# Performance work log

Hardware: AMD Instinct MI355X
Metric: run time of the kernel (lower is better)

Reference implementation:

```python
import jax, jax.numpy as jnp
import numpy as np
from jax import lax
from jax.scipy.special import logsumexp

TRIGGER_SIZE = 34
NTAG = TRIGGER_SIZE + 2  # +START/STOP
START = TRIGGER_SIZE
STOP = TRIGGER_SIZE + 1


def setup_inputs() -> dict:
    key = jax.random.key(0)
    k1, k2, k3, k4, k5 = jax.random.split(key, 5)
    B, S, H = 64, 512, 768
    x_1 = jax.random.normal(k1, (B, S, H), dtype=jnp.float32)
    head_indexes = jax.random.randint(k2, (B, S), 0, S)
    triggers_y = jax.random.randint(k3, (B, S), 0, TRIGGER_SIZE)
    W = jax.random.normal(k4, (H, NTAG), dtype=jnp.float32) * (1.0 / np.sqrt(H))
    b = jnp.zeros((NTAG,), dtype=jnp.float32)
    transitions = jax.random.normal(k5, (NTAG, NTAG), dtype=jnp.float32) * 0.1
    return {"x_1": x_1, "head_indexes": head_indexes, "triggers_y": triggers_y,
            "W": W, "b": b, "transitions": transitions}


def crf_nll(emit, mask, tags, trans):
    # emit [B,S,T], mask [B,S] bool, tags [B,S], trans [T,T] (from->to)
    B, S, T = emit.shape
    maskf = mask.astype(emit.dtype)
    # --- partition (forward algorithm) ---
    alpha0 = emit[:, 0] + trans[START][None, :]  # [B,T]; pos 0 always valid

    def fstep(alpha, inp):
        e_t, m_t = inp  # [B,T], [B]
        new = logsumexp(alpha[:, :, None] + trans[None, :, :], axis=1) + e_t
        return jnp.where(m_t[:, None], new, alpha), None

    alpha, _ = lax.scan(fstep, alpha0,
                        (emit[:, 1:].transpose(1, 0, 2), mask[:, 1:].T))
    logZ = logsumexp(alpha + trans[:, STOP][None, :], axis=1)  # [B]
    # --- gold path score ---
    emit_g = jnp.take_along_axis(emit, tags[:, :, None], axis=2)[..., 0]  # [B,S]
    emit_score = (emit_g * maskf).sum(axis=1)
    trans_pair = trans[tags[:, :-1], tags[:, 1:]]  # [B,S-1]
    trans_score = (trans_pair * maskf[:, 1:]).sum(axis=1)
    xlen = mask.sum(axis=1)  # [B]
    last_tag = jnp.take_along_axis(tags, (xlen - 1)[:, None], axis=1)[:, 0]
    gold = emit_score + trans[START, tags[:, 0]] + trans_score + trans[last_tag, STOP]
    return jnp.sum(logZ - gold)


def crf_viterbi(emit, mask, trans):
    B, S, T = emit.shape
    ids = jnp.arange(T)
    delta0 = emit[:, 0] + trans[START][None, :]

    def vstep(delta, inp):
        e_t, m_t = inp
        scores = delta[:, :, None] + trans[None, :, :]  # [B,T,T]
        best = scores.max(axis=1) + e_t
        bp = jnp.argmax(scores, axis=1)  # [B,T]
        new_delta = jnp.where(m_t[:, None], best, delta)
        bp = jnp.where(m_t[:, None], bp, ids[None, :])  # identity on pad
        return new_delta, bp

    delta, bps = lax.scan(vstep, delta0,
                          (emit[:, 1:].transpose(1, 0, 2), mask[:, 1:].T))
    final = delta + trans[:, STOP][None, :]
    last_tag = jnp.argmax(final, axis=1)  # [B]
    path_score = jnp.max(final, axis=1)

    def back(tag_next, bp_t):
        tag_t = jnp.take_along_axis(bp_t, tag_next[:, None], axis=1)[:, 0]
        return tag_t, tag_t

    _, prev_tags = lax.scan(back, last_tag, bps, reverse=True)  # [S-1,B]
    path = jnp.concatenate([prev_tags.T, last_tag[:, None]], axis=1)  # [B,S]
    path = jnp.where(mask, path, 0)
    return path_score, path


def reference(x_1, head_indexes, triggers_y, W, b, transitions):
    B, S, H = x_1.shape
    # batched version of the per-sample index_select loop
    x = jnp.take_along_axis(x_1, head_indexes[:, :, None], axis=1)  # [B,S,H]
    xlen = head_indexes.max(axis=1)  # xlen = [max(row) for row in head_indexes]
    mask = jnp.arange(S)[None, :] < xlen[:, None]  # [B,S] bool
    logits = jax.nn.leaky_relu(x @ W + b)  # tri_fc1 + leaky_relu (dropout=eval)
    trigger_loss = crf_nll(logits, mask, triggers_y, transitions)
    path_score, trigger_hat = crf_viterbi(logits, mask, transitions)
    return trigger_loss, trigger_hat, path_score
```

## Files before the change

kernel.cpp:

```cpp
#include <hip/hip_runtime.h>
#include <math.h>

#define SB 64
#define SS 512
#define SH 768
#define NT 36
#define TSTART 34
#define TSTOP 35
#define NC 32
#define CL 16

#define CFENCE() asm volatile("" ::: "memory")

__device__ __forceinline__ float wave_max_f(float v) {
#pragma unroll
    for (int off = 32; off > 0; off >>= 1) v = fmaxf(v, __shfl_xor(v, off, 64));
    return v;
}
__device__ __forceinline__ float wave_sum_f(float v) {
#pragma unroll
    for (int off = 32; off > 0; off >>= 1) v += __shfl_xor(v, off, 64);
    return v;
}
__device__ __forceinline__ float bcast0(float v) {
    return __uint_as_float(__builtin_amdgcn_readfirstlane(__float_as_uint(v)));
}

#define XP 129
#define XBUF 8256
#define RED(qq, rr, jj) smem[(qq) * 2368 + (rr) * 37 + (jj)]

extern "C" __global__ __launch_bounds__(512) void k_emit(
    const float* __restrict__ x1, const int* __restrict__ hidx,
    const float* __restrict__ W, const float* __restrict__ bias,
    float* __restrict__ emit)
{
    __shared__ __align__(16) float smem[18944];

    int tid  = threadIdx.x;
    int lane = tid & 63;
    int q    = __builtin_amdgcn_readfirstlane(tid >> 6);

    int srow = tid >> 3;
    int c8   = tid & 7;
    int grs  = blockIdx.x * 64 + srow;
    int bs   = grs >> 9;
    const float4* srcRow = (const float4*)(x1 + (size_t)(bs * SS + hidx[grs]) * SH);
    int woff = srow * XP + c8 * 4;

    float acc[NT];
#pragma unroll
    for (int j = 0; j < NT; ++j) acc[j] = 0.f;

    float4 n0, n1, n2, n3;
    n0 = srcRow[c8];  n1 = srcRow[c8 + 8];
    n2 = srcRow[c8 + 16]; n3 = srcRow[c8 + 24];
    {
        float* d = smem + woff;
        d[0] = n0.x; d[1] = n0.y; d[2] = n0.z; d[3] = n0.w;
        d[32] = n1.x; d[33] = n1.y; d[34] = n1.z; d[35] = n1.w;
        d[64] = n2.x; d[65] = n2.y; d[66] = n2.z; d[67] = n2.w;
        d[96] = n3.x; d[97] = n3.y; d[98] = n3.z; d[99] = n3.w;
    }

#pragma unroll
    for (int s = 0; s < 6; ++s) {
        if (s < 5) {
            int f0 = (s + 1) * 32 + c8;
            n0 = srcRow[f0]; n1 = srcRow[f0 + 8];
            n2 = srcRow[f0 + 16]; n3 = srcRow[f0 + 24];
        }
        __syncthreads();
        {
            const float* xs = smem + (s & 1) * XBUF + lane * XP + 16 * q;
            const float* Ws = W + (size_t)(128 * s + 16 * q) * NT;
#pragma unroll
            for (int k = 0; k < 16; ++k) {
                float xv = xs[k];
                const float* wr = Ws + k * NT;
#pragma unroll
                for (int j = 0; j < NT; ++j) acc[j] += xv * wr[j];
            }
        }
        if (s < 5) {
            float* d = smem + ((s + 1) & 1) * XBUF + woff;
            d[0] = n0.x; d[1] = n0.y; d[2] = n0.z; d[3] = n0.w;
            d[32] = n1.x; d[33] = n1.y; d[34] = n1.z; d[35] = n1.w;
            d[64] = n2.x; d[65] = n2.y; d[66] = n2.z; d[67] = n2.w;
            d[96] = n3.x; d[97] = n3.y; d[98] = n3.z; d[99] = n3.w;
        }
    }
    __syncthreads();

#pragma unroll
    for (int j = 0; j < NT; ++j) RED(q, lane, j) = acc[j];
    __syncthreads();

    int r = tid >> 2, g = tid & 3;
    float vout[9];
    if (tid < 256) {
#pragma unroll
        for (int jj = 0; jj < 9; ++jj) {
            int j = g * 9 + jj;
            float v = bias[j];
#pragma unroll
            for (int qq = 0; qq < 8; ++qq) v += RED(qq, r, j);
            vout[jj] = v > 0.f ? v : 0.01f * v;
        }
    }
    __syncthreads();
    if (tid < 256) {
#pragma unroll
        for (int jj = 0; jj < 9; ++jj) smem[r * NT + g * 9 + jj] = vout[jj];
    }
    __syncthreads();
    {
        const float4* st4 = (const float4*)smem;
        float4* op = (float4*)(emit + (size_t)blockIdx.x * 64 * NT);
        for (int i = tid; i < 576; i += 512) op[i] = st4[i];
    }
}

#define LSE_STEP(T)                                                       \
    {                                                                     \
        float e_t = elsw[((T) - t0s) * NT + jj];                          \
        float m = bcast0(alpha);                                          \
        float p = __expf(alpha - m);                                      \
        bc[lane] = p;                                                     \
        CFENCE();                                                         \
        __builtin_amdgcn_wave_barrier();                                  \
        float s0 = 0.f, s1 = 0.f, s2 = 0.f, s3 = 0.f;                     \
        _Pragma("unroll")                                                 \
        for (int k = 0; k < 9; ++k) {                                     \
            float4 pv = bc4[w][k];                                        \
            s0 += pv.x * Ecol[4 * k];                                     \
            s1 += pv.y * Ecol[4 * k + 1];                                 \
            s2 += pv.z * Ecol[4 * k + 2];                                 \
            s3 += pv.w * Ecol[4 * k + 3];                                 \
        }                                                                 \
        CFENCE();                                                         \
        float anew = m + __logf((s0 + s1) + (s2 + s3)) + e_t;             \
        alpha = act ? anew : -1e30f;                                      \
    }

#define VIT_STEP(T, WRITEBP)                                              \
    {                                                                     \
        float e_t = elsw[((T) - t0s) * NT + jj];                          \
        bc[lane] = alpha;                                                 \
        CFENCE();                                                         \
        __builtin_amdgcn_wave_barrier();                                  \
        float b0 = -1e30f, b1 = -1e30f, b2 = -1e30f, b3 = -1e30f;         \
        int   i0 = 0, i1 = 1, i2 = 2, i3 = 3;                             \
        _Pragma("unroll")                                                 \
        for (int k = 0; k < 9; ++k) {                                     \
            float4 dv = bc4[w][k];                                        \
            float c0 = dv.x + tcol[4 * k];                                 \
            float c1 = dv.y + tcol[4 * k + 1];                             \
            float c2 = dv.z + tcol[4 * k + 2];                             \
            float c3 = dv.w + tcol[4 * k + 3];                             \
            if (c0 > b0) { b0 = c0; i0 = 4 * k; }                         \
            if (c1 > b1) { b1 = c1; i1 = 4 * k + 1; }                     \
            if (c2 > b2) { b2 = c2; i2 = 4 * k + 2; }                     \
            if (c3 > b3) { b3 = c3; i3 = 4 * k + 3; }                     \
        }                                                                 \
        CFENCE();                                                         \
        float best = b0; int bi = i0;                                     \
        if (b1 > best || (b1 == best && i1 < bi)) { best = b1; bi = i1; } \
        if (b2 > best || (b2 == best && i2 < bi)) { best = b2; bi = i2; } \
        if (b3 > best || (b3 == best && i3 < bi)) { best = b3; bi = i3; } \
        float dnew = best + e_t;                                          \
        alpha = act ? dnew : -1e30f;                                      \
        if ((WRITEBP) && act)                                             \
            bp[((size_t)b * SS + (T)) * 64 + jj] = (unsigned char)bi;     \
    }

extern "C" __global__ __launch_bounds__(256) void k_scan(
    const float* __restrict__ emit, const int* __restrict__ hidx,
    const float* __restrict__ trans,
    float* __restrict__ Warr, float* __restrict__ Earr,
    float* __restrict__ lse_local,
    float* __restrict__ score_local, int* __restrict__ ltag,
    unsigned char* __restrict__ bp)
{
    __shared__ float trl[NT * NT];
    __shared__ float els[4][1024];
    __shared__ float4 bc4[4][16];

    int tid  = threadIdx.x;
    int lane = tid & 63;
    int w    = __builtin_amdgcn_readfirstlane(tid >> 6);

    int wid  = blockIdx.x * 4 + w;
    int kind = wid >> 11;
    int rem  = wid & 2047;
    int b    = rem >> 5;
    int c    = rem & 31;

    const float* eb  = emit + (size_t)b * SS * NT;
    int t0s = (c > 0) ? (c * CL - 9) : 0;
    const float* ebase = eb + (size_t)t0s * NT;
    float* elsw = els[w];

#pragma unroll
    for (int i = 0; i < 4; ++i) {
        __builtin_amdgcn_global_load_lds(
            (const __attribute__((address_space(1))) void*)(ebase + i * 256 + lane * 4),
            (__attribute__((address_space(3))) void*)(elsw + i * 256), 16, 0, 0);
    }
    for (int i = tid; i < NT * NT; i += 256) trl[i] = trans[i];

    int  jj  = lane < NT ? lane : NT - 1;
    bool act = lane < NT;

    int xm = 0;
    const int* hb = hidx + b * SS;
#pragma unroll
    for (int k = 0; k < SS / 64; ++k) xm = max(xm, hb[lane + 64 * k]);
#pragma unroll
    for (int off = 32; off > 0; off >>= 1) xm = max(xm, __shfl_xor(xm, off, 64));
    int xlen = xm;
    int cl   = (xlen >= 1) ? ((xlen - 1) >> 4) : 0;

    int tb0 = c * CL - 8;
    int te0 = c * CL; if (te0 > xlen) te0 = xlen; te0 -= 1;
    int tb  = c * CL; if (tb < 1) tb = 1;
    int te  = (c + 1) * CL; if (te > xlen) te = xlen; te -= 1;

    int didx = (kind * SB + b) * NC + c;

    float alpha;
    if (c == 0) alpha = act ? (eb[jj] + trans[TSTART * NT + jj]) : -1e30f;
    else        alpha = act ? eb[(size_t)(tb0 - 1) * NT + jj] : -1e30f;

    __syncthreads();

    float* bc = (float*)bc4[w];

    if (kind == 0) {
        float Ecol[NT];
#pragma unroll
        for (int i = 0; i < NT; ++i) Ecol[i] = __expf(trl[i * NT + jj]);
        if (c > 0) {
            for (int t = tb0; t <= te0; ++t) LSE_STEP(t)
        }
        float Wv = bcast0(alpha);
        for (int t = tb; t <= te; ++t) LSE_STEP(t)
        float Ev = bcast0(alpha);
        if (lane == 0) { Warr[didx] = Wv; Earr[didx] = Ev; }
        if (c == cl) {
            float ff = act ? (alpha + trl[jj * NT + TSTOP]) : -1e30f;
            float M = wave_max_f(ff);
            float ssum = wave_sum_f(__expf(ff - M));
            if (lane == 0) lse_local[b] = M + __logf(ssum);
        }
    } else {
        float tcol[NT];
#pragma unroll
        for (int i = 0; i < NT; ++i) tcol[i] = trl[i * NT + jj];
        if (c > 0) {
            for (int t = tb0; t <= te0; ++t) VIT_STEP(t, 0)
        }
        float Wv = bcast0(alpha);
        for (int t = tb; t <= te; ++t) VIT_STEP(t, 1)
        float Ev = bcast0(alpha);
        if (lane == 0) { Warr[didx] = Wv; Earr[didx] = Ev; }
        if (c == cl) {
            float ff = act ? (alpha + trl[jj * NT + TSTOP]) : -1e30f;
            float bv = ff; int bi = lane;
#pragma unroll
            for (int off = 32; off > 0; off >>= 1) {
                float ov = __shfl_xor(bv, off, 64);
                int   oi = __shfl_xor(bi, off, 64);
                if (ov > bv || (ov == bv && oi < bi)) { bv = ov; bi = oi; }
            }
            if (lane == 0) { score_local[b] = bv; ltag[b] = bi; }
        }
    }
}

extern "C" __global__ __launch_bounds__(1024) void k_final(
    const float* __restrict__ emit, const int* __restrict__ hidx,
    const int* __restrict__ tags, const float* __restrict__ trans,
    const float* __restrict__ Warr, const float* __restrict__ Earr,
    const float* __restrict__ lse_local,
    const float* __restrict__ score_local, const int* __restrict__ ltag,
    const unsigned char* __restrict__ bp,
    float* __restrict__ loss_out, float* __restrict__ path_out,
    float* __restrict__ score_out)
{
    __shared__ unsigned char bpl[SS * 64];
    __shared__ unsigned char cmap[SS][40];
    __shared__ unsigned char exitmap[NC][64];
    __shared__ float gred[16];
    __shared__ int   ent[NC];

    int tid  = threadIdx.x;
    int lane = tid & 63;
    int w    = tid >> 6;
    int b    = blockIdx.x;

    {
        const int4* src = (const int4*)(bp + (size_t)b * SS * 64);
        int4* dst = (int4*)bpl;
        for (int i = tid; i < SS * 4; i += 1024) dst[i] = src[i];
    }

    int xm = 0;
    const int* hb = hidx + b * SS;
#pragma unroll
    for (int k = 0; k < SS / 64; ++k) xm = max(xm, hb[lane + 64 * k]);
#pragma unroll
    for (int off = 32; off > 0; off >>= 1) xm = max(xm, __shfl_xor(xm, off, 64));
    int xlen = xm;
    int cl   = (xlen >= 1) ? ((xlen - 1) >> 4) : 0;

    float g = 0.f;
    const int* tg = tags + b * SS;
    if (tid < SS) {
        int t = tid;
        if (t < xlen) {
            int tt = tg[t];
            g += emit[((size_t)b * SS + t) * NT + tt];
            if (t >= 1) g += trans[tg[t - 1] * NT + tt];
        }
    }
    g = wave_sum_f(g);
    if (lane == 0) gred[w] = g;

    float kf = 0.f, kv = 0.f;
    if (w == 8) {
        if (lane < cl) {
            kf = Earr[(0 * SB + b) * NC + lane] - Warr[(0 * SB + b) * NC + lane + 1];
            kv = Earr[(1 * SB + b) * NC + lane] - Warr[(1 * SB + b) * NC + lane + 1];
        }
        kf = wave_sum_f(kf);
        kv = wave_sum_f(kv);
    }

    __syncthreads();

    if (tid == 512) {
        float gold = 0.f;
#pragma unroll
        for (int i = 0; i < 8; ++i) gold += gred[i];
        int tg0 = tg[0];
        int lt  = (xlen >= 1) ? tg[xlen - 1] : tg0;
        gold += trans[TSTART * NT + tg0] + trans[lt * NT + TSTOP];
        atomicAdd(loss_out, (lse_local[b] + kf) - gold);
        score_out[b] = score_local[b] + kv;
    }

    for (int cc = 0; cc < 2; ++cc) {
        int c = w * 2 + cc;
        if (xlen >= 1 && c <= cl) {
            int tb = (c == 0) ? 1 : c * CL;
            int te = c * CL + CL - 1; if (te > xlen - 1) te = xlen - 1;
            int m = lane;
            if (lane < NT) cmap[te][lane] = (unsigned char)m;
            for (int t = te; t >= tb; --t) {
                m = bpl[t * 64 + m];
                if (lane < NT) {
                    if (t > tb || c == 0) cmap[t - 1][lane] = (unsigned char)m;
                    else                  exitmap[c][lane]  = (unsigned char)m;
                }
            }
        }
    }
    __syncthreads();

    if (tid == 0 && xlen >= 1) {
        int e = ltag[b];
        for (int c2 = cl; c2 >= 0; --c2) {
            ent[c2] = e;
            if (c2 > 0) e = exitmap[c2][e];
        }
    }
    __syncthreads();

    if (tid < SS) {
        int t = tid;
        float* op = path_out + (size_t)b * SS;
        if (t >= xlen) op[t] = 0.f;
        else           op[t] = (float)cmap[t][ent[t >> 4]];
    }
}

extern "C" void kernel_launch(void* const* d_in, const int* in_sizes, int n_in,
                              void* d_out, int out_size, void* d_ws, size_t ws_size,
                              hipStream_t stream)
{
    const float* x1    = (const float*)d_in[0];
    const int*   hidx  = (const int*)d_in[1];
    const int*   tags  = (const int*)d_in[2];
    const float* W     = (const float*)d_in[3];
    const float* bias  = (const float*)d_in[4];
    const float* trans = (const float*)d_in[5];
    float* out = (float*)d_out;

    float* emit        = (float*)d_ws;
    float* Warr        = emit + (size_t)SB * SS * NT;
    float* Earr        = Warr + 2 * SB * NC;
    float* lse_local   = Earr + 2 * SB * NC;
    float* score_local = lse_local + SB;
    int*   ltag        = (int*)(score_local + SB);
    float* spacer      = (float*)(ltag + SB);
    unsigned char* bp  = (unsigned char*)(spacer + SB);

    hipLaunchKernelGGL(k_emit, dim3(SB * SS / 64), dim3(512), 0, stream,
                       x1, hidx, W, bias, emit);
    hipLaunchKernelGGL(k_scan, dim3(1024), dim3(256), 0, stream,
                       emit, hidx, trans, Warr, Earr, lse_local,
                       score_local, ltag, bp);
    hipLaunchKernelGGL(k_final, dim3(SB), dim3(1024), 0, stream,
                       emit, hidx, tags, trans, Warr, Earr, lse_local,
                       score_local, ltag, bp, out, out + 1, out + 1 + SB * SS);
}
```

Measured before the change: 220.2 us.

## Fuse forward-algorithm and Viterbi chunk scans into one wave per chunk

```diff
diff --git a/kernel.cpp b/kernel.cpp
--- a/kernel.cpp
+++ b/kernel.cpp
@@ -121,55 +121,42 @@
     }
 }
 
-#define LSE_STEP(T)                                                       \
+#define STEP2(T, WRITEBP)                                                 \
     {                                                                     \
         float e_t = elsw[((T) - t0s) * NT + jj];                          \
-        float m = bcast0(alpha);                                          \
-        float p = __expf(alpha - m);                                      \
-        bc[lane] = p;                                                     \
+        float mL = bcast0(aL);                                            \
+        bcL[lane] = __expf(aL - mL);                                      \
+        bcV[lane] = aV;                                                   \
         CFENCE();                                                         \
         __builtin_amdgcn_wave_barrier();                                  \
         float s0 = 0.f, s1 = 0.f, s2 = 0.f, s3 = 0.f;                     \
+        float b0 = -1e30f, b1 = -1e30f, b2 = -1e30f, b3 = -1e30f;         \
+        int   i0 = 0, i1 = 1, i2 = 2, i3 = 3;                             \
         _Pragma("unroll")                                                 \
         for (int k = 0; k < 9; ++k) {                                     \
-            float4 pv = bc4[w][k];                                        \
+            float4 pv = bcL4[w][k];                                       \
+            float4 dv = bcV4[w][k];                                       \
             s0 += pv.x * Ecol[4 * k];                                     \
             s1 += pv.y * Ecol[4 * k + 1];                                 \
             s2 += pv.z * Ecol[4 * k + 2];                                 \
             s3 += pv.w * Ecol[4 * k + 3];                                 \
-        }                                                                 \
-        CFENCE();                                                         \
-        float anew = m + __logf((s0 + s1) + (s2 + s3)) + e_t;             \
-        alpha = act ? anew : -1e30f;                                      \
-    }
-
-#define VIT_STEP(T, WRITEBP)                                              \
-    {                                                                     \
-        float e_t = elsw[((T) - t0s) * NT + jj];                          \
-        bc[lane] = alpha;                                                 \
-        CFENCE();                                                         \
-        __builtin_amdgcn_wave_barrier();                                  \
-        float b0 = -1e30f, b1 = -1e30f, b2 = -1e30f, b3 = -1e30f;         \
-        int   i0 = 0, i1 = 1, i2 = 2, i3 = 3;                             \
-        _Pragma("unroll")                                                 \
-        for (int k = 0; k < 9; ++k) {                                     \
-            float4 dv = bc4[w][k];                                        \
-            float c0 = dv.x + tcol[4 * k];                                 \
-            float c1 = dv.y + tcol[4 * k + 1];                             \
-            float c2 = dv.z + tcol[4 * k + 2];                             \
-            float c3 = dv.w + tcol[4 * k + 3];                             \
+            float c0 = dv.x + tcol[4 * k];                                \
+            float c1 = dv.y + tcol[4 * k + 1];                            \
+            float c2 = dv.z + tcol[4 * k + 2];                            \
+            float c3 = dv.w + tcol[4 * k + 3];                            \
             if (c0 > b0) { b0 = c0; i0 = 4 * k; }                         \
             if (c1 > b1) { b1 = c1; i1 = 4 * k + 1; }                     \
             if (c2 > b2) { b2 = c2; i2 = 4 * k + 2; }                     \
             if (c3 > b3) { b3 = c3; i3 = 4 * k + 3; }                     \
         }                                                                 \
         CFENCE();                                                         \
+        float anewL = mL + __logf((s0 + s1) + (s2 + s3)) + e_t;           \
         float best = b0; int bi = i0;                                     \
         if (b1 > best || (b1 == best && i1 < bi)) { best = b1; bi = i1; } \
         if (b2 > best || (b2 == best && i2 < bi)) { best = b2; bi = i2; } \
         if (b3 > best || (b3 == best && i3 < bi)) { best = b3; bi = i3; } \
-        float dnew = best + e_t;                                          \
-        alpha = act ? dnew : -1e30f;                                      \
+        aL = act ? anewL : -1e30f;                                        \
+        aV = act ? (best + e_t) : -1e30f;                                 \
         if ((WRITEBP) && act)                                             \
             bp[((size_t)b * SS + (T)) * 64 + jj] = (unsigned char)bi;     \
     }
@@ -184,17 +171,16 @@
 {
     __shared__ float trl[NT * NT];
     __shared__ float els[4][1024];
-    __shared__ float4 bc4[4][16];
+    __shared__ float4 bcL4[4][16];
+    __shared__ float4 bcV4[4][16];
 
     int tid  = threadIdx.x;
     int lane = tid & 63;
     int w    = __builtin_amdgcn_readfirstlane(tid >> 6);
 
     int wid  = blockIdx.x * 4 + w;
-    int kind = wid >> 11;
-    int rem  = wid & 2047;
-    int b    = rem >> 5;
-    int c    = rem & 31;
+    int b    = wid >> 5;
+    int c    = wid & 31;
 
     const float* eb  = emit + (size_t)b * SS * NT;
     int t0s = (c > 0) ? (c * CL - 9) : 0;
@@ -226,55 +212,52 @@
     int tb  = c * CL; if (tb < 1) tb = 1;
     int te  = (c + 1) * CL; if (te > xlen) te = xlen; te -= 1;
 
-    int didx = (kind * SB + b) * NC + c;
-
-    float alpha;
-    if (c == 0) alpha = act ? (eb[jj] + trans[TSTART * NT + jj]) : -1e30f;
-    else        alpha = act ? eb[(size_t)(tb0 - 1) * NT + jj] : -1e30f;
-
-    __syncthreads();
-
-    float* bc = (float*)bc4[w];
-
-    if (kind == 0) {
-        float Ecol[NT];
-#pragma unroll
-        for (int i = 0; i < NT; ++i) Ecol[i] = __expf(trl[i * NT + jj]);
-        if (c > 0) {
-            for (int t = tb0; t <= te0; ++t) LSE_STEP(t)
-        }
-        float Wv = bcast0(alpha);
-        for (int t = tb; t <= te; ++t) LSE_STEP(t)
-        float Ev = bcast0(alpha);
-        if (lane == 0) { Warr[didx] = Wv; Earr[didx] = Ev; }
-        if (c == cl) {
-            float ff = act ? (alpha + trl[jj * NT + TSTOP]) : -1e30f;
-            float M = wave_max_f(ff);
-            float ssum = wave_sum_f(__expf(ff - M));
-            if (lane == 0) lse_local[b] = M + __logf(ssum);
-        }
-    } else {
-        float tcol[NT];
-#pragma unroll
-        for (int i = 0; i < NT; ++i) tcol[i] = trl[i * NT + jj];
-        if (c > 0) {
-            for (int t = tb0; t <= te0; ++t) VIT_STEP(t, 0)
-        }
-        float Wv = bcast0(alpha);
-        for (int t = tb; t <= te; ++t) VIT_STEP(t, 1)
-        float Ev = bcast0(alpha);
-        if (lane == 0) { Warr[didx] = Wv; Earr[didx] = Ev; }
-        if (c == cl) {
-            float ff = act ? (alpha + trl[jj * NT + TSTOP]) : -1e30f;
-            float bv = ff; int bi = lane;
-#pragma unroll
-            for (int off = 32; off > 0; off >>= 1) {
-                float ov = __shfl_xor(bv, off, 64);
-                int   oi = __shfl_xor(bi, off, 64);
-                if (ov > bv || (ov == bv && oi < bi)) { bv = ov; bi = oi; }
-            }
-            if (lane == 0) { score_local[b] = bv; ltag[b] = bi; }
-        }
+    float init;
+    if (c == 0) init = act ? (eb[jj] + trans[TSTART * NT + jj]) : -1e30f;
+    else        init = act ? eb[(size_t)(tb0 - 1) * NT + jj] : -1e30f;
+    float aL = init, aV = init;
+
+    __syncthreads();
+
+    float* bcL = (float*)bcL4[w];
+    float* bcV = (float*)bcV4[w];
+
+    float tcol[NT], Ecol[NT];
+#pragma unroll
+    for (int i = 0; i < NT; ++i) {
+        tcol[i] = trl[i * NT + jj];
+        Ecol[i] = __expf(tcol[i]);
+    }
+
+    if (c > 0) {
+        for (int t = tb0; t <= te0; ++t) STEP2(t, 0)
+    }
+    float WvL = bcast0(aL), WvV = bcast0(aV);
+    for (int t = tb; t <= te; ++t) STEP2(t, 1)
+    float EvL = bcast0(aL), EvV = bcast0(aV);
+
+    if (lane == 0) {
+        Warr[b * NC + c]        = WvL;
+        Earr[b * NC + c]        = EvL;
+        Warr[(SB + b) * NC + c] = WvV;
+        Earr[(SB + b) * NC + c] = EvV;
+    }
+
+    if (c == cl) {
+        float ffL = act ? (aL + trl[jj * NT + TSTOP]) : -1e30f;
+        float M = wave_max_f(ffL);
+        float ssum = wave_sum_f(__expf(ffL - M));
+        if (lane == 0) lse_local[b] = M + __logf(ssum);
+
+        float ffV = act ? (aV + trl[jj * NT + TSTOP]) : -1e30f;
+        float bv = ffV; int bi = lane;
+#pragma unroll
+        for (int off = 32; off > 0; off >>= 1) {
+            float ov = __shfl_xor(bv, off, 64);
+            int   oi = __shfl_xor(bi, off, 64);
+            if (ov > bv || (ov == bv && oi < bi)) { bv = ov; bi = oi; }
+        }
+        if (lane == 0) { score_local[b] = bv; ltag[b] = bi; }
     }
 }
 
@@ -408,7 +391,7 @@
 
     hipLaunchKernelGGL(k_emit, dim3(SB * SS / 64), dim3(512), 0, stream,
                        x1, hidx, W, bias, emit);
-    hipLaunchKernelGGL(k_scan, dim3(1024), dim3(256), 0, stream,
+    hipLaunchKernelGGL(k_scan, dim3(512), dim3(256), 0, stream,
                        emit, hidx, trans, Warr, Earr, lse_local,
                        score_local, ltag, bp);
     hipLaunchKernelGGL(k_final, dim3(SB), dim3(1024), 0, stream,
```

Result: no change. 222.2 us (+0.9%).
